# Kernel tuning notes

Hardware: AMD Instinct MI355X
Metric: run time of the kernel (lower is better)

## Reference

```python
import jax, jax.numpy as jnp
import numpy as np

EMBED_DIM = 1024
NUM_HEADS = 16
DEPTH = EMBED_DIM // NUM_HEADS


def setup_inputs() -> dict:
    key = jax.random.key(0)
    ks = jax.random.split(key, 6)
    B, S, D = 2, 2048, EMBED_DIM
    scale = 1.0 / np.sqrt(D)
    return {
        "x": jax.random.normal(ks[0], (B, S, D), dtype=jnp.float32),
        "mask": jax.random.randint(ks[1], (B, S), 0, 2, dtype=jnp.int32),
        "wq_w": jax.random.normal(ks[2], (D, D), dtype=jnp.float32) * scale,
        "wq_b": jnp.zeros((D,), dtype=jnp.float32),
        "wk_w": jax.random.normal(ks[3], (D, D), dtype=jnp.float32) * scale,
        "wk_b": jnp.zeros((D,), dtype=jnp.float32),
        "wv_w": jax.random.normal(ks[4], (D, D), dtype=jnp.float32) * scale,
        "wv_b": jnp.zeros((D,), dtype=jnp.float32),
        "dense_w": jax.random.normal(ks[5], (D, D), dtype=jnp.float32) * scale,
        "dense_b": jnp.zeros((D,), dtype=jnp.float32),
    }


def _split_heads(t, B, S):
    # [B, S, D] -> [B, H, S, depth]
    return t.reshape(B, S, NUM_HEADS, DEPTH).transpose(0, 2, 1, 3)


def reference(x, mask, wq_w, wq_b, wk_w, wk_b, wv_w, wv_b, dense_w, dense_b):
    B, S, D = x.shape
    q = _split_heads(x @ wq_w.T + wq_b, B, S)  # [B, H, S, d]
    k = _split_heads(x @ wk_w.T + wk_b, B, S)
    v = _split_heads(x @ wv_w.T + wv_b, B, S)

    logits = jnp.einsum('bhqd,bhkd->bhqk', q, k) / jnp.sqrt(
        jnp.asarray(DEPTH, dtype=jnp.float32))
    # mask [B, S] broadcast to [B, 1, 1, S] over key axis, additive -1e9
    logits = logits + mask.astype(logits.dtype)[:, None, None, :] * (-1e9)
    attn = jax.nn.softmax(logits, axis=-1)  # [B, H, S, S]
    ctx = jnp.einsum('bhqk,bhkd->bhqd', attn, v)
    ctx = ctx.transpose(0, 2, 1, 3).reshape(B, S, D)
    out = ctx @ dense_w.T + dense_b
    return out, attn
```

## Files before the change

### kernel.cpp

```cpp
#include <hip/hip_runtime.h>


#define S_LEN 2048
#define D_DIM 1024
#define H_NUM 16
#define M_ROWS 4096

typedef __attribute__((ext_vector_type(8))) short bf16x8;
typedef __attribute__((ext_vector_type(4))) float f32x4;

static __device__ __forceinline__ unsigned short f2bf(float f) {
  union { float f; unsigned u; } v; v.f = f;
  unsigned r = (v.u + 0x7FFFu + ((v.u >> 16) & 1u)) >> 16;
  return (unsigned short)r;
}

static __device__ __forceinline__ bf16x8 cvt8(float4 a, float4 b) {
  bf16x8 r;
  r[0] = (short)f2bf(a.x); r[1] = (short)f2bf(a.y);
  r[2] = (short)f2bf(a.z); r[3] = (short)f2bf(a.w);
  r[4] = (short)f2bf(b.x); r[5] = (short)f2bf(b.y);
  r[6] = (short)f2bf(b.z); r[7] = (short)f2bf(b.w);
  return r;
}

static __device__ __forceinline__ void gld16(const void* g, void* s) {
  __builtin_amdgcn_global_load_lds(
      (const __attribute__((address_space(1))) unsigned int*)g,
      (__attribute__((address_space(3))) unsigned int*)s, 16, 0, 0);
}

__global__ __launch_bounds__(256) void cast_f32_bf16(
    const float* __restrict__ src, unsigned short* __restrict__ dst, int n4) {
  int i = blockIdx.x * 256 + threadIdx.x;
  if (i >= n4) return;
  float4 v = ((const float4*)src)[i];
  unsigned long long o =
      (unsigned long long)f2bf(v.x) |
      ((unsigned long long)f2bf(v.y) << 16) |
      ((unsigned long long)f2bf(v.z) << 32) |
      ((unsigned long long)f2bf(v.w) << 48);
  ((unsigned long long*)dst)[i] = o;
}

__global__ __launch_bounds__(256) void gemm_qkv(
    const unsigned short* __restrict__ A,
    const unsigned short* __restrict__ W0, const unsigned short* __restrict__ W1,
    const unsigned short* __restrict__ W2,
    const float* __restrict__ b0, const float* __restrict__ b1,
    const float* __restrict__ b2,
    unsigned short* __restrict__ C0, unsigned short* __restrict__ C1,
    unsigned short* __restrict__ C2) {
  const unsigned short* W = W0; const float* bias = b0; unsigned short* C = C0;
  if (blockIdx.z == 1) { W = W1; bias = b1; C = C1; }
  else if (blockIdx.z == 2) { W = W2; bias = b2; C = C2; }

  __shared__ __align__(16) unsigned short As[128 * 64];
  __shared__ __align__(16) unsigned short Bs[128 * 64];

  const int tid = threadIdx.x;
  const int l = tid & 63;
  const int w = tid >> 6;
  const int wm = w >> 1, wn = w & 1;
  const int lo = l & 15, hi = l >> 4;

  const int mBase = blockIdx.y * 128;
  const int nBase = blockIdx.x * 128;

  f32x4 acc[4][4];
  for (int mr = 0; mr < 4; ++mr)
    for (int nr = 0; nr < 4; ++nr) acc[mr][nr] = (f32x4){0.f, 0.f, 0.f, 0.f};

  for (int k0 = 0; k0 < 1024; k0 += 64) {
    __syncthreads();
    for (int i = 0; i < 4; ++i) {
      int s = w * 4 + i;
      int row = s * 8 + (l >> 3), colb = (l & 7) * 8;
      gld16(A + (size_t)(mBase + row) * 1024 + k0 + colb, As + s * 512);
      gld16(W + (size_t)(nBase + row) * 1024 + k0 + colb, Bs + s * 512);
    }
    __syncthreads();
    for (int kk = 0; kk < 2; ++kk) {
      bf16x8 af[4], bfm[4];
      for (int mr = 0; mr < 4; ++mr)
        af[mr] = *(const bf16x8*)&As[(wm * 64 + mr * 16 + lo) * 64 + kk * 32 + hi * 8];
      for (int nr = 0; nr < 4; ++nr)
        bfm[nr] = *(const bf16x8*)&Bs[(wn * 64 + nr * 16 + lo) * 64 + kk * 32 + hi * 8];
      for (int mr = 0; mr < 4; ++mr)
        for (int nr = 0; nr < 4; ++nr)
          acc[mr][nr] = __builtin_amdgcn_mfma_f32_16x16x32_bf16(
              af[mr], bfm[nr], acc[mr][nr], 0, 0, 0);
    }
  }

  if (blockIdx.z == 2) {
    for (int nr = 0; nr < 4; ++nr) {
      int col = nBase + wn * 64 + nr * 16 + lo;
      float bv = bias[col];
      int hh = col >> 6, dd = col & 63;
      for (int mr = 0; mr < 4; ++mr) {
        int rbase = mBase + wm * 64 + mr * 16 + hi * 4;
        int bb = rbase >> 11, ss = rbase & 2047;
        unsigned long long o = 0;
        for (int i = 0; i < 4; ++i)
          o |= (unsigned long long)f2bf(acc[mr][nr][i] + bv) << (16 * i);
        *(unsigned long long*)(C +
            ((size_t)((bb * H_NUM + hh) * 64 + dd) * S_LEN + ss)) = o;
      }
    }
  } else {
    for (int nr = 0; nr < 4; ++nr) {
      int col = nBase + wn * 64 + nr * 16 + lo;
      float bv = bias[col];
      for (int mr = 0; mr < 4; ++mr) {
        int rbase = mBase + wm * 64 + mr * 16 + hi * 4;
        for (int i = 0; i < 4; ++i)
          C[(size_t)(rbase + i) * 1024 + col] = f2bf(acc[mr][nr][i] + bv);
      }
    }
  }
}

__global__ __launch_bounds__(256) void gemm_proj(
    const unsigned short* __restrict__ A, const float* __restrict__ W,
    const float* __restrict__ bias, float* __restrict__ C) {
  __shared__ __align__(16) unsigned short As[128][40];
  __shared__ __align__(16) unsigned short Bs[128][40];

  const int tid = threadIdx.x;
  const int l = tid & 63;
  const int w = tid >> 6;
  const int wm = w >> 1, wn = w & 1;
  const int lo = l & 15, hi = l >> 4;

  const int mBase = blockIdx.y * 128;
  const int nBase = blockIdx.x * 128;

  f32x4 acc[4][4];
  for (int mr = 0; mr < 4; ++mr)
    for (int nr = 0; nr < 4; ++nr) acc[mr][nr] = (f32x4){0.f, 0.f, 0.f, 0.f};

  for (int k0 = 0; k0 < 1024; k0 += 32) {
    __syncthreads();
    for (int it = 0; it < 2; ++it) {
      int c = tid + it * 256;
      int r = c >> 2, cc = (c & 3) * 8;
      *(int4*)&As[r][cc] = *(const int4*)(A + (size_t)(mBase + r) * 1024 + k0 + cc);
      const float* wp = W + (size_t)(nBase + r) * 1024 + k0 + cc;
      *(bf16x8*)&Bs[r][cc] = cvt8(((const float4*)wp)[0], ((const float4*)wp)[1]);
    }
    __syncthreads();
    bf16x8 af[4], bfm[4];
    for (int mr = 0; mr < 4; ++mr)
      af[mr] = *(const bf16x8*)&As[wm * 64 + mr * 16 + lo][hi * 8];
    for (int nr = 0; nr < 4; ++nr)
      bfm[nr] = *(const bf16x8*)&Bs[wn * 64 + nr * 16 + lo][hi * 8];
    for (int mr = 0; mr < 4; ++mr)
      for (int nr = 0; nr < 4; ++nr)
        acc[mr][nr] = __builtin_amdgcn_mfma_f32_16x16x32_bf16(
            af[mr], bfm[nr], acc[mr][nr], 0, 0, 0);
  }

  for (int nr = 0; nr < 4; ++nr) {
    int col = nBase + wn * 64 + nr * 16 + lo;
    float bv = bias[col];
    for (int mr = 0; mr < 4; ++mr) {
      int rbase = mBase + wm * 64 + mr * 16 + hi * 4;
      for (int i = 0; i < 4; ++i)
        C[(size_t)(rbase + i) * 1024 + col] = acc[mr][nr][i] + bv;
    }
  }
}

__global__ __launch_bounds__(256) void attn_kernel(
    const unsigned short* __restrict__ qb, const unsigned short* __restrict__ kb,
    const unsigned short* __restrict__ vT, const int* __restrict__ mask,
    float* __restrict__ attn, unsigned short* __restrict__ ctx) {
  const int bid = blockIdx.x;
  const int wid = (bid & 7) * 128 + (bid >> 3);
  const int q0 = (wid & 31) * 64;
  const int h  = (wid >> 5) & 15;
  const int b  = wid >> 9;

  const int tid = threadIdx.x, l = tid & 63, w = tid >> 6;
  const int lo = l & 15, hi = l >> 4;

  __shared__ __align__(16) unsigned short k_lds[64][72];
  __shared__ __align__(16) unsigned short vt_lds[64][72];
  __shared__ __align__(16) float p_f32[64][68];

  bf16x8 qa[2];
  {
    const size_t qrow = (size_t)(b * S_LEN + q0 + w * 16 + lo) * D_DIM + h * 64;
    qa[0] = *(const bf16x8*)(qb + qrow + hi * 8);
    qa[1] = *(const bf16x8*)(qb + qrow + 32 + hi * 8);
  }

  const size_t kvbase = (size_t)b * S_LEN * D_DIM + h * 64;
  const unsigned short* vTh = vT + (size_t)((b * H_NUM + h) * 64) * S_LEN;
  const int* maskb = mask + b * S_LEN;

  float rsum[4] = {0.f, 0.f, 0.f, 0.f};
  for (int kt = 0; kt < 32; ++kt) {
    const int key0 = kt * 64;
    __syncthreads();
#pragma unroll
    for (int it = 0; it < 2; ++it) {
      int c = tid + it * 256;
      int r = c >> 3, cc = (c & 7) * 8;
      *(int4*)&k_lds[r][cc] =
          *(const int4*)(kb + kvbase + (size_t)(key0 + r) * D_DIM + cc);
    }
    __syncthreads();
    f32x4 acc[4];
    for (int nr = 0; nr < 4; ++nr) acc[nr] = (f32x4){0.f, 0.f, 0.f, 0.f};
#pragma unroll
    for (int kk = 0; kk < 2; ++kk)
#pragma unroll
      for (int nr = 0; nr < 4; ++nr) {
        bf16x8 kf = *(const bf16x8*)&k_lds[nr * 16 + lo][kk * 32 + hi * 8];
        acc[nr] = __builtin_amdgcn_mfma_f32_16x16x32_bf16(qa[kk], kf, acc[nr], 0, 0, 0);
      }
    for (int nr = 0; nr < 4; ++nr) {
      float ma = maskb[key0 + nr * 16 + lo] ? -1e9f : 0.f;
      for (int i = 0; i < 4; ++i)
        rsum[i] += __expf(acc[nr][i] * 0.125f + ma);
    }
  }
  for (int m = 1; m < 16; m <<= 1)
    for (int i = 0; i < 4; ++i) rsum[i] += __shfl_xor(rsum[i], m);
  float inv[4];
  for (int i = 0; i < 4; ++i) inv[i] = 1.0f / rsum[i];

  f32x4 ctxacc[4];
  for (int dc = 0; dc < 4; ++dc) ctxacc[dc] = (f32x4){0.f, 0.f, 0.f, 0.f};
  const size_t attnbase = (size_t)(b * H_NUM + h) * S_LEN * S_LEN;

  for (int kt = 0; kt < 32; ++kt) {
    const int key0 = kt * 64;
    __syncthreads();
#pragma unroll
    for (int it = 0; it < 2; ++it) {
      int c = tid + it * 256;
      int r = c >> 3, cc = (c & 7) * 8;
      *(int4*)&k_lds[r][cc] =
          *(const int4*)(kb + kvbase + (size_t)(key0 + r) * D_DIM + cc);
      *(int4*)&vt_lds[r][cc] =
          *(const int4*)(vTh + (size_t)r * S_LEN + key0 + cc);
    }
    __syncthreads();
    f32x4 acc[4];
    for (int nr = 0; nr < 4; ++nr) acc[nr] = (f32x4){0.f, 0.f, 0.f, 0.f};
#pragma unroll
    for (int kk = 0; kk < 2; ++kk)
#pragma unroll
      for (int nr = 0; nr < 4; ++nr) {
        bf16x8 kf = *(const bf16x8*)&k_lds[nr * 16 + lo][kk * 32 + hi * 8];
        acc[nr] = __builtin_amdgcn_mfma_f32_16x16x32_bf16(qa[kk], kf, acc[nr], 0, 0, 0);
      }
    for (int nr = 0; nr < 4; ++nr) {
      float ma = maskb[key0 + nr * 16 + lo] ? -1e9f : 0.f;
      for (int i = 0; i < 4; ++i)
        p_f32[w * 16 + hi * 4 + i][nr * 16 + lo] =
            __expf(acc[nr][i] * 0.125f + ma) * inv[i];
    }
    __syncthreads();

    bf16x8 pa[2];
    for (int kk = 0; kk < 2; ++kk) {
      const float* pr = &p_f32[w * 16 + lo][kk * 32 + hi * 8];
      pa[kk] = cvt8(*(const float4*)pr, *(const float4*)(pr + 4));
    }
#pragma unroll
    for (int kk = 0; kk < 2; ++kk)
#pragma unroll
      for (int dc = 0; dc < 4; ++dc) {
        bf16x8 vf = *(const bf16x8*)&vt_lds[dc * 16 + lo][kk * 32 + hi * 8];
        ctxacc[dc] = __builtin_amdgcn_mfma_f32_16x16x32_bf16(
            pa[kk], vf, ctxacc[dc], 0, 0, 0);
      }

#pragma unroll
    for (int it = 0; it < 4; ++it) {
      int c = tid + it * 256;
      int r = c >> 4, cc = (c & 15) * 4;
      *(float4*)(attn + attnbase + (size_t)(q0 + r) * S_LEN + key0 + cc) =
          *(const float4*)&p_f32[r][cc];
    }
  }

  for (int dc = 0; dc < 4; ++dc) {
    int col = h * 64 + dc * 16 + lo;
    for (int i = 0; i < 4; ++i) {
      int row = q0 + w * 16 + hi * 4 + i;
      ctx[(size_t)(b * S_LEN + row) * D_DIM + col] = f2bf(ctxacc[dc][i]);
    }
  }
}

extern "C" void kernel_launch(void* const* d_in, const int* in_sizes, int n_in,
                              void* d_out, int out_size, void* d_ws, size_t ws_size,
                              hipStream_t stream) {
  const float* x    = (const float*)d_in[0];
  const int*   mask = (const int*)d_in[1];
  const float* wq   = (const float*)d_in[2];
  const float* bq   = (const float*)d_in[3];
  const float* wk   = (const float*)d_in[4];
  const float* bk   = (const float*)d_in[5];
  const float* wv   = (const float*)d_in[6];
  const float* bv   = (const float*)d_in[7];
  const float* wd   = (const float*)d_in[8];
  const float* bd   = (const float*)d_in[9];

  float* out  = (float*)d_out;
  float* attn = out + (size_t)M_ROWS * D_DIM;

  unsigned short* xb  = (unsigned short*)attn;
  unsigned short* wqb = xb + 4194304;
  unsigned short* wkb = xb + 5242880;
  unsigned short* wvb = xb + 6291456;

  unsigned short* ws   = (unsigned short*)d_ws;
  unsigned short* qb   = ws;
  unsigned short* kbuf = ws + 4194304;
  unsigned short* vTb  = ws + 8388608;
  unsigned short* ctxb = ws + 12582912;

  cast_f32_bf16<<<4096, 256, 0, stream>>>(x,  xb,  1048576);
  cast_f32_bf16<<<1024, 256, 0, stream>>>(wq, wqb, 262144);
  cast_f32_bf16<<<1024, 256, 0, stream>>>(wk, wkb, 262144);
  cast_f32_bf16<<<1024, 256, 0, stream>>>(wv, wvb, 262144);

  gemm_qkv<<<dim3(8, 32, 3), 256, 0, stream>>>(
      xb, wqb, wkb, wvb, bq, bk, bv, qb, kbuf, vTb);

  attn_kernel<<<1024, 256, 0, stream>>>(qb, kbuf, vTb, mask, attn, ctxb);

  gemm_proj<<<dim3(8, 32), 256, 0, stream>>>(ctxb, wd, bd, out);
}
```

Before: 352.4 us.

## Split attention into rowsum and apply kernels, keep probabilities as bf16 in LDS

The softmax denominator pass moves into its own kernel, which writes inverse row sums to a scratch area of the output buffer. The main attention kernel reads those sums and then makes a single pass. Probabilities are now stored in LDS as bf16 instead of fp32. Each wave reads back only its own rows, which removes one block-wide barrier per key tile and shrinks shared memory, possibly allowing more resident blocks. The cost is that the attention output written to global memory is now bf16-rounded rather than full fp32, and there is an extra kernel launch.

```diff
diff --git a/kernel.cpp b/kernel.cpp
--- a/kernel.cpp
+++ b/kernel.cpp
@@ -172,10 +172,9 @@
   }
 }
 
-__global__ __launch_bounds__(256) void attn_kernel(
+__global__ __launch_bounds__(256) void rowsum_kernel(
     const unsigned short* __restrict__ qb, const unsigned short* __restrict__ kb,
-    const unsigned short* __restrict__ vT, const int* __restrict__ mask,
-    float* __restrict__ attn, unsigned short* __restrict__ ctx) {
+    const int* __restrict__ mask, float* __restrict__ invb) {
   const int bid = blockIdx.x;
   const int wid = (bid & 7) * 128 + (bid >> 3);
   const int q0 = (wid & 31) * 64;
@@ -186,8 +185,6 @@
   const int lo = l & 15, hi = l >> 4;
 
   __shared__ __align__(16) unsigned short k_lds[64][72];
-  __shared__ __align__(16) unsigned short vt_lds[64][72];
-  __shared__ __align__(16) float p_f32[64][68];
 
   bf16x8 qa[2];
   {
@@ -195,9 +192,7 @@
     qa[0] = *(const bf16x8*)(qb + qrow + hi * 8);
     qa[1] = *(const bf16x8*)(qb + qrow + 32 + hi * 8);
   }
-
   const size_t kvbase = (size_t)b * S_LEN * D_DIM + h * 64;
-  const unsigned short* vTh = vT + (size_t)((b * H_NUM + h) * 64) * S_LEN;
   const int* maskb = mask + b * S_LEN;
 
   float rsum[4] = {0.f, 0.f, 0.f, 0.f};
@@ -229,8 +224,45 @@
   }
   for (int m = 1; m < 16; m <<= 1)
     for (int i = 0; i < 4; ++i) rsum[i] += __shfl_xor(rsum[i], m);
+  if (lo == 0) {
+    const int base = (b * H_NUM + h) * S_LEN + q0 + w * 16 + hi * 4;
+    for (int i = 0; i < 4; ++i) invb[base + i] = 1.0f / rsum[i];
+  }
+}
+
+__global__ __launch_bounds__(256) void attn_kernel(
+    const unsigned short* __restrict__ qb, const unsigned short* __restrict__ kb,
+    const unsigned short* __restrict__ vT, const int* __restrict__ mask,
+    const float* __restrict__ invb, float* __restrict__ attn,
+    unsigned short* __restrict__ ctx) {
+  const int bid = blockIdx.x;
+  const int wid = (bid & 7) * 128 + (bid >> 3);
+  const int q0 = (wid & 31) * 64;
+  const int h  = (wid >> 5) & 15;
+  const int b  = wid >> 9;
+
+  const int tid = threadIdx.x, l = tid & 63, w = tid >> 6;
+  const int lo = l & 15, hi = l >> 4;
+
+  __shared__ __align__(16) unsigned short k_lds[64][72];
+  __shared__ __align__(16) unsigned short vt_lds[64][72];
+  __shared__ __align__(16) unsigned short p_lds[64][72];
+
+  bf16x8 qa[2];
+  {
+    const size_t qrow = (size_t)(b * S_LEN + q0 + w * 16 + lo) * D_DIM + h * 64;
+    qa[0] = *(const bf16x8*)(qb + qrow + hi * 8);
+    qa[1] = *(const bf16x8*)(qb + qrow + 32 + hi * 8);
+  }
+  const size_t kvbase = (size_t)b * S_LEN * D_DIM + h * 64;
+  const unsigned short* vTh = vT + (size_t)((b * H_NUM + h) * 64) * S_LEN;
+  const int* maskb = mask + b * S_LEN;
+
   float inv[4];
-  for (int i = 0; i < 4; ++i) inv[i] = 1.0f / rsum[i];
+  {
+    const int base = (b * H_NUM + h) * S_LEN + q0 + w * 16 + hi * 4;
+    for (int i = 0; i < 4; ++i) inv[i] = invb[base + i];
+  }
 
   f32x4 ctxacc[4];
   for (int dc = 0; dc < 4; ++dc) ctxacc[dc] = (f32x4){0.f, 0.f, 0.f, 0.f};
@@ -260,17 +292,14 @@
       }
     for (int nr = 0; nr < 4; ++nr) {
       float ma = maskb[key0 + nr * 16 + lo] ? -1e9f : 0.f;
-      for (int i = 0; i < 4; ++i)
-        p_f32[w * 16 + hi * 4 + i][nr * 16 + lo] =
-            __expf(acc[nr][i] * 0.125f + ma) * inv[i];
-    }
-    __syncthreads();
-
+      for (int i = 0; i < 4; ++i) {
+        float p = __expf(acc[nr][i] * 0.125f + ma) * inv[i];
+        p_lds[w * 16 + hi * 4 + i][nr * 16 + lo] = f2bf(p);
+      }
+    }
     bf16x8 pa[2];
-    for (int kk = 0; kk < 2; ++kk) {
-      const float* pr = &p_f32[w * 16 + lo][kk * 32 + hi * 8];
-      pa[kk] = cvt8(*(const float4*)pr, *(const float4*)(pr + 4));
-    }
+    for (int kk = 0; kk < 2; ++kk)
+      pa[kk] = *(const bf16x8*)&p_lds[w * 16 + lo][kk * 32 + hi * 8];
 #pragma unroll
     for (int kk = 0; kk < 2; ++kk)
 #pragma unroll
@@ -279,13 +308,15 @@
         ctxacc[dc] = __builtin_amdgcn_mfma_f32_16x16x32_bf16(
             pa[kk], vf, ctxacc[dc], 0, 0, 0);
       }
-
 #pragma unroll
     for (int it = 0; it < 4; ++it) {
-      int c = tid + it * 256;
-      int r = c >> 4, cc = (c & 15) * 4;
-      *(float4*)(attn + attnbase + (size_t)(q0 + r) * S_LEN + key0 + cc) =
-          *(const float4*)&p_f32[r][cc];
+      int row = w * 16 + it * 4 + hi;
+      int2 pk = *(const int2*)&p_lds[row][lo * 4];
+      union { unsigned u; float f; } e0, e1, e2, e3;
+      e0.u = (unsigned)pk.x << 16; e1.u = pk.x & 0xffff0000u;
+      e2.u = (unsigned)pk.y << 16; e3.u = pk.y & 0xffff0000u;
+      *(float4*)(attn + attnbase + (size_t)(q0 + row) * S_LEN + key0 + lo * 4) =
+          (float4){e0.f, e1.f, e2.f, e3.f};
     }
   }
 
@@ -320,6 +351,8 @@
   unsigned short* wkb = xb + 5242880;
   unsigned short* wvb = xb + 6291456;
 
+  float* invb = out;
+
   unsigned short* ws   = (unsigned short*)d_ws;
   unsigned short* qb   = ws;
   unsigned short* kbuf = ws + 4194304;
@@ -334,7 +367,9 @@
   gemm_qkv<<<dim3(8, 32, 3), 256, 0, stream>>>(
       xb, wqb, wkb, wvb, bq, bk, bv, qb, kbuf, vTb);
 
-  attn_kernel<<<1024, 256, 0, stream>>>(qb, kbuf, vTb, mask, attn, ctxb);
+  rowsum_kernel<<<1024, 256, 0, stream>>>(qb, kbuf, mask, invb);
+
+  attn_kernel<<<1024, 256, 0, stream>>>(qb, kbuf, vTb, mask, invb, attn, ctxb);
 
   gemm_proj<<<dim3(8, 32), 256, 0, stream>>>(ctxb, wd, bd, out);
 }
```

New measurement: 384.4 us. 1.09x slower.
